# Kernel tuning notes

Measured on AMD Instinct MI355X. Metric: run time of the kernel, lower is better.

## Reference

```python
import jax, jax.numpy as jnp
import numpy as np

EMBED_DIM = 1024
NUM_HEADS = 16
HEAD_DIM = EMBED_DIM // NUM_HEADS
BSZ = 4
SEQ = 1500


def setup_inputs() -> dict:
    key = jax.random.key(0)
    ks = jax.random.split(key, 8)
    s = 0.02
    return {
        "hidden_states": jax.random.normal(ks[0], (BSZ, SEQ, EMBED_DIM), jnp.float32),
        "Wq": jax.random.normal(ks[1], (EMBED_DIM, EMBED_DIM), jnp.float32) * s,
        "bq": jax.random.normal(ks[2], (EMBED_DIM,), jnp.float32) * s,
        "Wk": jax.random.normal(ks[3], (EMBED_DIM, EMBED_DIM), jnp.float32) * s,
        "Wv": jax.random.normal(ks[4], (EMBED_DIM, EMBED_DIM), jnp.float32) * s,
        "bv": jax.random.normal(ks[5], (EMBED_DIM,), jnp.float32) * s,
        "Wo": jax.random.normal(ks[6], (EMBED_DIM, EMBED_DIM), jnp.float32) * s,
        "bo": jax.random.normal(ks[7], (EMBED_DIM,), jnp.float32) * s,
    }


def reference(hidden_states, Wq, bq, Wk, Wv, bv, Wo, bo):
    b, t, e = hidden_states.shape
    h, d = NUM_HEADS, HEAD_DIM
    scaling = d ** -0.5

    def shape(x):  # [b, t, e] -> [b, h, t, d]
        return x.reshape(b, t, h, d).transpose(0, 2, 1, 3)

    # q_proj (with bias) then scale applied to the full projected output,
    # matching the original (scale multiplies q_proj output incl. bias).
    q = shape((hidden_states @ Wq.T + bq) * scaling)
    k = shape(hidden_states @ Wk.T)            # k_proj has no bias in Whisper
    v = shape(hidden_states @ Wv.T + bv)

    # naive materialized attention scores: [b, h, t, t]
    attn_weights = jnp.einsum("bhqd,bhkd->bhqk", q, k)
    attn_probs = jax.nn.softmax(attn_weights, axis=-1)
    attn_output = jnp.einsum("bhqk,bhkd->bhqd", attn_probs, v)

    # [b, h, t, d] -> [b, t, e]
    attn_output = attn_output.transpose(0, 2, 1, 3).reshape(b, t, e)
    return attn_output @ Wo.T + bo
```

## Files before the change

kernel.cpp:

```cpp
#include <hip/hip_runtime.h>
#include <math.h>

#define E 1024
#define NH 16
#define HD 64
#define BSZ_ 4
#define SEQ_ 1500
#define VSTR 1504
#define M_ (BSZ_ * SEQ_)
#define SZE ((size_t)M_ * (size_t)E)
#define QSC (0.125f * 1.44269504f)

#define QA_OFF  0u
#define XB_OFF  6144000u
#define WB_OFF  12288000u
#define WOB_OFF 15433728u
#define VT_OFF  16482304u
#define CVT_TOTAL 10338304u
#define PAD_ELEMS 18432u
#define WS_FAST_BYTES 45289472ull

typedef __attribute__((ext_vector_type(8))) short short8v;
typedef __attribute__((ext_vector_type(4))) float f32x4;
typedef __attribute__((ext_vector_type(16))) float f32x16;
typedef __attribute__((ext_vector_type(4))) unsigned short ushort4v;

__device__ __forceinline__ unsigned short f2bf(float f) {
    union { float f; unsigned int i; } c; c.f = f;
    return (unsigned short)((c.i + 0x7FFFu + ((c.i >> 16) & 1u)) >> 16);
}
__device__ __forceinline__ unsigned int cvt_pk_bf16(float a, float b) {
    unsigned int r;
    asm("v_cvt_pk_bf16_f32 %0, %1, %2" : "=v"(r) : "v"(a), "v"(b));
    return r;
}
__device__ __forceinline__ void perml32(unsigned int &a, unsigned int &b) {
    asm("v_permlane32_swap_b32 %0, %1" : "+v"(a), "+v"(b));
}

__device__ __forceinline__ int swz(int row, int col) {
    return (row << 6) + ((((col >> 3) ^ row) & 7) << 3) + (col & 7);
}
__device__ __forceinline__ int swzf(int r, int d) {
    int row = r >> 1;
    int cs = ((r & 1) << 3) | (d >> 3);
    return row * 128 + ((cs ^ (row & 15)) << 3) + (d & 7);
}

__device__ __forceinline__ short8v pack8(const float* x) {
    union { unsigned int u[4]; short8v v; } r;
    r.u[0] = cvt_pk_bf16(x[0], x[1]);
    r.u[1] = cvt_pk_bf16(x[2], x[3]);
    r.u[2] = cvt_pk_bf16(x[4], x[5]);
    r.u[3] = cvt_pk_bf16(x[6], x[7]);
    return r.v;
}

__device__ __forceinline__ void gload16(const unsigned short* g,
                                        unsigned short* l) {
    __builtin_amdgcn_global_load_lds(
        (const __attribute__((address_space(1))) unsigned int*)(g),
        (__attribute__((address_space(3))) unsigned int*)(l), 16, 0, 0);
}

__global__ __launch_bounds__(256) void cvt_kernel(
    const float* __restrict__ X,  const float* __restrict__ Wk,
    const float* __restrict__ Wv, const float* __restrict__ Wq,
    const float* __restrict__ Wo, unsigned short* __restrict__ ws)
{
    size_t w = ((size_t)blockIdx.x * 256 + threadIdx.x) * 8;
    if (w >= CVT_TOTAL) {
        size_t p0 = w - CVT_TOTAL;
        unsigned short* Vt = ws + VT_OFF;
#pragma unroll
        for (int i = 0; i < 8; ++i) {
            size_t e = p0 + i;
            if (e < 16384u) {
                size_t row = e >> 2;
                Vt[row * VSTR + 1500 + (e & 3)] = 0;
            } else if (e < PAD_ELEMS) {
                Vt[(size_t)4096 * VSTR + (e - 16384u)] = 0;
            }
        }
        return;
    }
    const float* s; unsigned short* d; float sc = 1.0f;
    if (w < 6144000u)      { s = X  + w;             d = ws + XB_OFF + w; }
    else if (w < 7192576u) { s = Wk + (w - 6144000u); d = ws + WB_OFF + (w - 6144000u); }
    else if (w < 8241152u) { s = Wv + (w - 7192576u); d = ws + WB_OFF + 1048576u + (w - 7192576u); }
    else if (w < 9289728u) { s = Wq + (w - 8241152u); d = ws + WB_OFF + 2097152u + (w - 8241152u); sc = QSC; }
    else                   { s = Wo + (w - 9289728u); d = ws + WOB_OFF + (w - 9289728u); }
    float t[8];
    *(float4*)t = *(const float4*)s;
    *(float4*)(t + 4) = *(const float4*)(s + 4);
#pragma unroll
    for (int i = 0; i < 8; ++i) t[i] *= sc;
    *(short8v*)d = pack8(t);
}

__device__ __forceinline__ void gemm128b(
    const unsigned short* __restrict__ Arow,
    const unsigned short* __restrict__ Brow,
    unsigned short* As, unsigned short* Bs, int tid, f32x4 acc[4][4])
{
    const int lane = tid & 63, wid = tid >> 6;
    const int wm = tid >> 7, wn = (tid >> 6) & 1;
    for (int k0 = 0; k0 < E; k0 += 64) {
#pragma unroll
        for (int i = 0; i < 4; ++i) {
            int row = wid * 32 + i * 8 + (lane >> 3);
            int sl = (lane & 7) ^ (row & 7);
            unsigned short* lbase = As + (wid * 32 + i * 8) * 64;
            gload16(Arow + (size_t)row * E + k0 + sl * 8, lbase);
            unsigned short* lbase2 = Bs + (wid * 32 + i * 8) * 64;
            gload16(Brow + (size_t)row * E + k0 + sl * 8, lbase2);
        }
        __syncthreads();
#pragma unroll
        for (int kk = 0; kk < 64; kk += 32) {
            short8v afr[4], bfr[4];
#pragma unroll
            for (int m = 0; m < 4; ++m)
                afr[m] = *(const short8v*)(As + swz(wm * 64 + m * 16 + (lane & 15),
                                                    kk + (lane >> 4) * 8));
#pragma unroll
            for (int n = 0; n < 4; ++n)
                bfr[n] = *(const short8v*)(Bs + swz(wn * 64 + n * 16 + (lane & 15),
                                                    kk + (lane >> 4) * 8));
            __builtin_amdgcn_s_setprio(1);
#pragma unroll
            for (int m = 0; m < 4; ++m)
#pragma unroll
                for (int n = 0; n < 4; ++n)
                    acc[m][n] = __builtin_amdgcn_mfma_f32_16x16x32_bf16(
                        afr[m], bfr[n], acc[m][n], 0, 0, 0);
            __builtin_amdgcn_s_setprio(0);
        }
        __syncthreads();
    }
}

__global__ __launch_bounds__(256) void proj_fast(
    const unsigned short* __restrict__ Xb, const unsigned short* __restrict__ Wb,
    const float* __restrict__ bv, const float* __restrict__ bq,
    unsigned short* __restrict__ Kb, unsigned short* __restrict__ Vt,
    unsigned short* __restrict__ Qa)
{
    __shared__ unsigned short As[128 * 64], Bs[128 * 64];
    const int sid = blockIdx.x;
    const int nid = (sid & 7) * 141 + (sid >> 3);
    const int mb = nid / 24, nb = nid % 24;
    const int z = nb >> 3;
    const size_t m0 = (size_t)mb * 128;
    const int tid = threadIdx.x, lane = tid & 63;
    const int wm = tid >> 7, wn = (tid >> 6) & 1;

    f32x4 acc[4][4];
#pragma unroll
    for (int m = 0; m < 4; ++m)
#pragma unroll
        for (int n = 0; n < 4; ++n)
#pragma unroll
            for (int i = 0; i < 4; ++i) acc[m][n][i] = 0.f;

    gemm128b(Xb + m0 * E, Wb + (size_t)nb * 128 * E, As, Bs, tid, acc);

#pragma unroll
    for (int m = 0; m < 4; ++m) {
        long gi0 = (long)m0 + wm * 64 + m * 16 + (lane >> 4) * 4;
#pragma unroll
        for (int n = 0; n < 4; ++n) {
            int col = (nb & 7) * 128 + wn * 64 + n * 16 + (lane & 15);
            if (z == 0) {
#pragma unroll
                for (int rg = 0; rg < 4; ++rg) {
                    long gi = gi0 + rg;
                    if (gi < M_) Kb[(size_t)gi * E + col] = f2bf(acc[m][n][rg]);
                }
            } else if (z == 2) {
                float bias = bq[col] * QSC;
#pragma unroll
                for (int rg = 0; rg < 4; ++rg) {
                    long gi = gi0 + rg;
                    if (gi < M_)
                        Qa[(size_t)gi * E + col] = f2bf(acc[m][n][rg] + bias);
                }
            } else {
                float bias = bv[col];
                if (gi0 + 3 < M_) {
                    long bb = gi0 / SEQ_, t0 = gi0 % SEQ_;
                    union { unsigned int u[2]; ushort4v v; } pk;
                    pk.u[0] = cvt_pk_bf16(acc[m][n][0] + bias, acc[m][n][1] + bias);
                    pk.u[1] = cvt_pk_bf16(acc[m][n][2] + bias, acc[m][n][3] + bias);
                    *(ushort4v*)(Vt + ((size_t)bb * E + col) * VSTR + t0) = pk.v;
                } else {
#pragma unroll
                    for (int rg = 0; rg < 4; ++rg) {
                        long gi = gi0 + rg;
                        if (gi < M_) {
                            long bb = gi / SEQ_, t = gi % SEQ_;
                            Vt[((size_t)bb * E + col) * VSTR + t] =
                                f2bf(acc[m][n][rg] + bias);
                        }
                    }
                }
            }
        }
    }
}

__global__ __launch_bounds__(256) void oproj_fast(
    const unsigned short* __restrict__ Ab, const unsigned short* __restrict__ Wob,
    const float* __restrict__ bo, float* __restrict__ out)
{
    __shared__ unsigned short As[128 * 64], Bs[128 * 64];
    const int sid = blockIdx.x;
    const int nid = (sid & 7) * 47 + (sid >> 3);
    const int mb = nid >> 3, nb = nid & 7;
    const size_t m0 = (size_t)mb * 128;
    const int tid = threadIdx.x, lane = tid & 63;
    const int wm = tid >> 7, wn = (tid >> 6) & 1;

    f32x4 acc[4][4];
#pragma unroll
    for (int m = 0; m < 4; ++m)
#pragma unroll
        for (int n = 0; n < 4; ++n)
#pragma unroll
            for (int i = 0; i < 4; ++i) acc[m][n][i] = 0.f;

    gemm128b(Ab + m0 * E, Wob + (size_t)nb * 128 * E, As, Bs, tid, acc);

#pragma unroll
    for (int m = 0; m < 4; ++m) {
        long gi0 = (long)m0 + wm * 64 + m * 16 + (lane >> 4) * 4;
#pragma unroll
        for (int n = 0; n < 4; ++n) {
            int col = nb * 128 + wn * 64 + n * 16 + (lane & 15);
            float bias = bo[col];
#pragma unroll
            for (int rg = 0; rg < 4; ++rg) {
                long gi = gi0 + rg;
                if (gi < M_) out[(size_t)gi * E + col] = acc[m][n][rg] + bias;
            }
        }
    }
}

__global__ __launch_bounds__(256, 4) void attn_gl(
    const unsigned short* __restrict__ Kb,
    const unsigned short* __restrict__ Vt,
    unsigned short* __restrict__ Qa)
{
    __shared__ unsigned short ks[4096], vs[4096];
    const int sid = blockIdx.x;
    const int nid = (sid & 7) * 96 + (sid >> 3);
    const int bh = nid / 12, qb = nid % 12;
    const int b = bh >> 4, hh = bh & 15;
    const int tid = threadIdx.x, lane = tid & 63, wz = tid >> 6;
    const int c = lane & 31, g2 = lane >> 5;
    const int q0 = qb * 128 + wz * 32;

    const unsigned short* kbase = Kb + (size_t)b * SEQ_ * E + hh * 64;
    const unsigned short* vbase = Vt + ((size_t)b * E + hh * 64) * VSTR;

    auto stageKV = [&](int kt0) {
#pragma unroll
        for (int i = 0; i < 2; ++i) {
            int j = (i * 4 + wz) * 64 + lane;
            int rp = j >> 4;
            int u = (j & 15) ^ (rp & 15);
            int r = rp * 2 + (u >> 3);
            int s = u & 7;
            gload16(kbase + (size_t)(kt0 + r) * E + s * 8,
                    ks + (i * 4 + wz) * 512);
            gload16(vbase + (size_t)r * VSTR + kt0 + s * 8,
                    vs + (i * 4 + wz) * 512);
        }
    };

    short8v qf[4];
    {
        int qr = q0 + c;
        bool ok = qr < SEQ_;
        const unsigned short* qp = Qa + ((size_t)b * SEQ_ + qr) * E + hh * 64 + 8 * g2;
#pragma unroll
        for (int t = 0; t < 4; ++t) {
            short8v zv;
#pragma unroll
            for (int i = 0; i < 8; ++i) zv[i] = 0;
            if (ok) zv = *(const short8v*)(qp + t * 16);
            qf[t] = zv;
        }
    }

    f32x16 o0, o1;
#pragma unroll
    for (int i = 0; i < 16; ++i) { o0[i] = 0.f; o1[i] = 0.f; }
    float lsum = 0.f;

    const int NT = (SEQ_ + 63) / 64;
    for (int it = 0; it < NT; ++it) {
        const int kt0 = it * 64;
        __syncthreads();
        stageKV(kt0);
        __syncthreads();
        const bool tail = (kt0 + 64 > SEQ_);

#pragma unroll
        for (int nt = 0; nt < 2; ++nt) {
            f32x16 s;
#pragma unroll
            for (int i = 0; i < 16; ++i) s[i] = 0.f;
            __builtin_amdgcn_s_setprio(1);
#pragma unroll
            for (int t = 0; t < 4; ++t) {
                short8v af = *(const short8v*)(ks + swzf(nt * 32 + c, t * 16 + 8 * g2));
                s = __builtin_amdgcn_mfma_f32_32x32x16_bf16(af, qf[t], s, 0, 0, 0);
            }
            __builtin_amdgcn_s_setprio(0);
            if (tail) {
#pragma unroll
                for (int r = 0; r < 16; ++r) {
                    int key = kt0 + nt * 32 + (r & 3) + 8 * (r >> 2) + 4 * g2;
                    if (key >= SEQ_) s[r] = -1e30f;
                }
            }
            unsigned int pk[8];
            float ls0 = 0.f, ls1 = 0.f;
#pragma unroll
            for (int h = 0; h < 8; ++h) {
                float p0 = __builtin_amdgcn_exp2f(s[2 * h]);
                float p1 = __builtin_amdgcn_exp2f(s[2 * h + 1]);
                if (h & 1) ls1 += p0 + p1; else ls0 += p0 + p1;
                pk[h] = cvt_pk_bf16(p0, p1);
            }
            lsum += ls0 + ls1;
            perml32(pk[0], pk[2]); perml32(pk[1], pk[3]);
            perml32(pk[4], pk[6]); perml32(pk[5], pk[7]);
            __builtin_amdgcn_s_setprio(1);
#pragma unroll
            for (int tau = 0; tau < 2; ++tau) {
                union { unsigned int ww[4]; short8v v; } pa;
                pa.ww[0] = pk[4 * tau + 0];
                pa.ww[1] = pk[4 * tau + 1];
                pa.ww[2] = pk[4 * tau + 2];
                pa.ww[3] = pk[4 * tau + 3];
                int t = nt * 2 + tau;
                short8v vb0 = *(const short8v*)(vs + swzf(0 + c, t * 16 + 8 * g2));
                short8v vb1 = *(const short8v*)(vs + swzf(32 + c, t * 16 + 8 * g2));
                o0 = __builtin_amdgcn_mfma_f32_32x32x16_bf16(pa.v, vb0, o0, 0, 0, 0);
                o1 = __builtin_amdgcn_mfma_f32_32x32x16_bf16(pa.v, vb1, o1, 0, 0, 0);
            }
            __builtin_amdgcn_s_setprio(0);
        }
    }

    lsum += __shfl_xor(lsum, 32, 64);
    __syncthreads();
    float* lf = (float*)ks + wz * 32;
    if (lane < 32) lf[c] = 1.0f / lsum;
#pragma unroll
    for (int r = 0; r < 16; ++r) {
        int ql = (r & 3) + 8 * (r >> 2) + 4 * g2;
        int tq = q0 + ql;
        if (tq < SEQ_) {
            float inv = lf[ql];
            unsigned short* op = Qa + ((size_t)b * SEQ_ + tq) * E + hh * 64;
            op[c] = f2bf(o0[r] * inv);
            op[32 + c] = f2bf(o1[r] * inv);
        }
    }
}

template <bool ABF>
__device__ __forceinline__ void gemm128(
    const float* __restrict__ Af, const unsigned short* __restrict__ Ab,
    size_t arow0, int avalid,
    const float* __restrict__ W, int wrow0,
    unsigned short* As, unsigned short* Bs,
    int tid, f32x4 acc[4][4])
{
    const int lane = tid & 63;
    const int wm = (tid >> 7), wn = (tid >> 6) & 1;
    float4 pA[8]; short8v pAb[4]; float4 pB[8];

    auto loadT = [&](int k0) {
#pragma unroll
        for (int uu = 0; uu < 4; ++uu) {
            int u = tid + uu * 256, row = u >> 3, sl = (u & 7) * 8;
            if constexpr (ABF) {
                short8v t;
#pragma unroll
                for (int i = 0; i < 8; ++i) t[i] = 0;
                if (row < avalid)
                    t = *(const short8v*)(Ab + (arow0 + row) * E + k0 + sl);
                pAb[uu] = t;
            } else {
                float4 x0 = make_float4(0.f, 0.f, 0.f, 0.f), x1 = x0;
                if (row < avalid) {
                    const float* p = Af + (arow0 + row) * (size_t)E + k0 + sl;
                    x0 = *(const float4*)p; x1 = *(const float4*)(p + 4);
                }
                pA[2 * uu] = x0; pA[2 * uu + 1] = x1;
            }
            const float* q = W + (size_t)(wrow0 + row) * E + k0 + sl;
            pB[2 * uu] = *(const float4*)q;
            pB[2 * uu + 1] = *(const float4*)(q + 4);
        }
    };
    auto commitT = [&]() {
#pragma unroll
        for (int uu = 0; uu < 4; ++uu) {
            int u = tid + uu * 256, row = u >> 3, sl = (u & 7) * 8;
            if constexpr (ABF) {
                *(short8v*)(As + swz(row, sl)) = pAb[uu];
            } else {
                float t[8];
                *(float4*)t = pA[2 * uu]; *(float4*)(t + 4) = pA[2 * uu + 1];
                *(short8v*)(As + swz(row, sl)) = pack8(t);
            }
            float t2[8];
            *(float4*)t2 = pB[2 * uu]; *(float4*)(t2 + 4) = pB[2 * uu + 1];
            *(short8v*)(Bs + swz(row, sl)) = pack8(t2);
        }
    };

    loadT(0);
    for (int k0 = 0; k0 < E; k0 += 64) {
        __syncthreads();
        commitT();
        __syncthreads();
        if (k0 + 64 < E) loadT(k0 + 64);
#pragma unroll
        for (int kk = 0; kk < 64; kk += 32) {
            short8v afr[4], bfr[4];
#pragma unroll
            for (int m = 0; m < 4; ++m)
                afr[m] = *(const short8v*)(As + swz(wm * 64 + m * 16 + (lane & 15),
                                                    kk + (lane >> 4) * 8));
#pragma unroll
            for (int n = 0; n < 4; ++n)
                bfr[n] = *(const short8v*)(Bs + swz(wn * 64 + n * 16 + (lane & 15),
                                                    kk + (lane >> 4) * 8));
            __builtin_amdgcn_s_setprio(1);
#pragma unroll
            for (int m = 0; m < 4; ++m)
#pragma unroll
                for (int n = 0; n < 4; ++n)
                    acc[m][n] = __builtin_amdgcn_mfma_f32_16x16x32_bf16(
                        afr[m], bfr[n], acc[m][n], 0, 0, 0);
            __builtin_amdgcn_s_setprio(0);
        }
    }
}

__global__ __launch_bounds__(256, 2) void proj_kernel(
    const float* __restrict__ X, const float* __restrict__ Wk,
    const float* __restrict__ Wv, const float* __restrict__ bv,
    const float* __restrict__ Wq, const float* __restrict__ bq,
    unsigned short* __restrict__ Kb, unsigned short* __restrict__ Vt,
    unsigned short* __restrict__ Qo)
{
    __shared__ unsigned short As[128 * 64], Bs[128 * 64];
    const int sid = blockIdx.x, cpx = gridDim.x >> 3;
    const int nid = (sid & 7) * cpx + (sid >> 3);
    const int mb = nid / 24, nb = nid % 24;
    const int z = nb >> 3, nbz = nb & 7;
    const size_t m0 = (size_t)mb * 128;
    const int avalid = (M_ - (int)m0) < 128 ? (M_ - (int)m0) : 128;
    const float* W = (z == 0) ? Wk : (z == 1) ? Wv : Wq;

    f32x4 acc[4][4];
#pragma unroll
    for (int m = 0; m < 4; ++m)
#pragma unroll
        for (int n = 0; n < 4; ++n)
#pragma unroll
            for (int i = 0; i < 4; ++i) acc[m][n][i] = 0.f;

    gemm128<false>(X, nullptr, m0, avalid, W, nbz * 128, As, Bs, threadIdx.x, acc);

    const int tid = threadIdx.x, lane = tid & 63;
    const int wm = (tid >> 7), wn = (tid >> 6) & 1;
#pragma unroll
    for (int m = 0; m < 4; ++m) {
        long gi0 = (long)m0 + wm * 64 + m * 16 + (lane >> 4) * 4;
#pragma unroll
        for (int n = 0; n < 4; ++n) {
            int col = nbz * 128 + wn * 64 + n * 16 + (lane & 15);
            if (z == 0) {
#pragma unroll
                for (int rg = 0; rg < 4; ++rg) {
                    long gi = gi0 + rg;
                    if (gi < M_) Kb[(size_t)gi * E + col] = f2bf(acc[m][n][rg]);
                }
            } else if (z == 2) {
                float bias = bq[col];
#pragma unroll
                for (int rg = 0; rg < 4; ++rg) {
                    long gi = gi0 + rg;
                    if (gi < M_)
                        Qo[(size_t)gi * E + col] = f2bf((acc[m][n][rg] + bias) * QSC);
                }
            } else {
                float bias = bv[col];
                if (gi0 + 3 < M_) {
                    long bb = gi0 / SEQ_, t0 = gi0 % SEQ_;
                    union { unsigned int u[2]; ushort4v v; } pk;
                    pk.u[0] = cvt_pk_bf16(acc[m][n][0] + bias, acc[m][n][1] + bias);
                    pk.u[1] = cvt_pk_bf16(acc[m][n][2] + bias, acc[m][n][3] + bias);
                    *(ushort4v*)(Vt + ((size_t)bb * E + col) * SEQ_ + t0) = pk.v;
                } else {
#pragma unroll
                    for (int rg = 0; rg < 4; ++rg) {
                        long gi = gi0 + rg;
                        if (gi < M_) {
                            long bb = gi / SEQ_, t = gi % SEQ_;
                            Vt[((size_t)bb * E + col) * SEQ_ + t] =
                                f2bf(acc[m][n][rg] + bias);
                        }
                    }
                }
            }
        }
    }
}

__global__ __launch_bounds__(256, 2) void oproj_kernel(
    const unsigned short* __restrict__ Ab, const float* __restrict__ Wo,
    const float* __restrict__ bo, float* __restrict__ out)
{
    __shared__ unsigned short As[128 * 64], Bs[128 * 64];
    const int sid = blockIdx.x, cpx = gridDim.x >> 3;
    const int nid = (sid & 7) * cpx + (sid >> 3);
    const int mb = nid >> 3, nb = nid & 7;
    const size_t m0 = (size_t)mb * 128;
    const int avalid = (M_ - (int)m0) < 128 ? (M_ - (int)m0) : 128;

    f32x4 acc[4][4];
#pragma unroll
    for (int m = 0; m < 4; ++m)
#pragma unroll
        for (int n = 0; n < 4; ++n)
#pragma unroll
            for (int i = 0; i < 4; ++i) acc[m][n][i] = 0.f;

    gemm128<true>(nullptr, Ab, m0, avalid, Wo, nb * 128, As, Bs, threadIdx.x, acc);

    const int tid = threadIdx.x, lane = tid & 63;
    const int wm = (tid >> 7), wn = (tid >> 6) & 1;
#pragma unroll
    for (int m = 0; m < 4; ++m) {
        long gi0 = (long)m0 + wm * 64 + m * 16 + (lane >> 4) * 4;
#pragma unroll
        for (int n = 0; n < 4; ++n) {
            int col = nb * 128 + wn * 64 + n * 16 + (lane & 15);
            float bias = bo[col];
#pragma unroll
            for (int rg = 0; rg < 4; ++rg) {
                long gi = gi0 + rg;
                if (gi < M_) out[(size_t)gi * E + col] = acc[m][n][rg] + bias;
            }
        }
    }
}

__global__ __launch_bounds__(256, 4) void attn_fallback(
    const unsigned short* __restrict__ Kb,
    const unsigned short* __restrict__ Vt,
    unsigned short* __restrict__ Qa)
{
    __shared__ unsigned short ks[2][32 * 128], vs[2][32 * 128];
    const int sid = blockIdx.x;
    const int nid = (sid & 7) * 96 + (sid >> 3);
    const int bh = nid / 12, qb = nid % 12;
    const int b = bh >> 4, hh = bh & 15;
    const int tid = threadIdx.x, lane = tid & 63, wz = tid >> 6;
    const int c = lane & 31, g2 = lane >> 5;
    const int q0 = qb * 128 + wz * 32;

    const unsigned short* kbase = Kb + (size_t)b * SEQ_ * E + hh * 64;
    const unsigned short* vbase = Vt + ((size_t)b * E + hh * 64) * SEQ_;

    short8v kreg[2];
    ushort4v vreg[4];
    auto loadK = [&](int kt0) {
#pragma unroll
        for (int uu = 0; uu < 2; ++uu) {
            int u = tid + uu * 256, key = u >> 3, slot = (u & 7) * 8;
            short8v t;
#pragma unroll
            for (int i = 0; i < 8; ++i) t[i] = 0;
            int gk = kt0 + key;
            if (gk < SEQ_) t = *(const short8v*)(kbase + (size_t)gk * E + slot);
            kreg[uu] = t;
        }
    };
    auto loadV = [&](int kt0) {
#pragma unroll
        for (int uu = 0; uu < 4; ++uu) {
            int u = tid + uu * 256, d = u >> 4, q4 = (u & 15) * 4;
            ushort4v t; t[0] = t[1] = t[2] = t[3] = 0;
            int col = kt0 + q4, rem = SEQ_ - col;
            const unsigned short* src = vbase + (size_t)d * SEQ_ + col;
            if (rem >= 4) t = *(const ushort4v*)src;
            else if (rem > 0) { for (int e2 = 0; e2 < 4; ++e2) if (e2 < rem) t[e2] = src[e2]; }
            vreg[uu] = t;
        }
    };
    auto commitKV = [&](unsigned short* kd, unsigned short* vd) {
#pragma unroll
        for (int uu = 0; uu < 2; ++uu) {
            int u = tid + uu * 256;
            *(short8v*)(kd + swzf(u >> 3, (u & 7) * 8)) = kreg[uu];
        }
#pragma unroll
        for (int uu = 0; uu < 4; ++uu) {
            int u = tid + uu * 256;
            *(ushort4v*)(vd + swzf(u >> 4, (u & 15) * 4)) = vreg[uu];
        }
    };

    loadK(0); loadV(0);

    short8v qf[4];
    {
        int qr = q0 + c;
        bool ok = qr < SEQ_;
        const unsigned short* qp = Qa + ((size_t)b * SEQ_ + qr) * E + hh * 64 + 8 * g2;
#pragma unroll
        for (int t = 0; t < 4; ++t) {
            short8v zv;
#pragma unroll
            for (int i = 0; i < 8; ++i) zv[i] = 0;
            if (ok) zv = *(const short8v*)(qp + t * 16);
            qf[t] = zv;
        }
    }

    f32x16 o0, o1;
#pragma unroll
    for (int i = 0; i < 16; ++i) { o0[i] = 0.f; o1[i] = 0.f; }
    float lsum = 0.f;

    commitKV(ks[0], vs[0]);
    __syncthreads();
    loadK(64); loadV(64);

    const int NT = (SEQ_ + 63) / 64;
    for (int it = 0; it < NT; ++it) {
        const int kt0 = it * 64;
        const unsigned short* kcur = ks[it & 1];
        const unsigned short* vcur = vs[it & 1];
        const bool tail = (kt0 + 64 > SEQ_);

#pragma unroll
        for (int nt = 0; nt < 2; ++nt) {
            f32x16 s;
#pragma unroll
            for (int i = 0; i < 16; ++i) s[i] = 0.f;
#pragma unroll
            for (int t = 0; t < 4; ++t) {
                short8v af = *(const short8v*)(kcur + swzf(nt * 32 + c, t * 16 + 8 * g2));
                s = __builtin_amdgcn_mfma_f32_32x32x16_bf16(af, qf[t], s, 0, 0, 0);
            }
            if (tail) {
#pragma unroll
                for (int r = 0; r < 16; ++r) {
                    int key = kt0 + nt * 32 + (r & 3) + 8 * (r >> 2) + 4 * g2;
                    if (key >= SEQ_) s[r] = -1e30f;
                }
            }
            unsigned int pk[8];
            float ls0 = 0.f, ls1 = 0.f;
#pragma unroll
            for (int h = 0; h < 8; ++h) {
                float p0 = __builtin_amdgcn_exp2f(s[2 * h]);
                float p1 = __builtin_amdgcn_exp2f(s[2 * h + 1]);
                if (h & 1) ls1 += p0 + p1; else ls0 += p0 + p1;
                pk[h] = cvt_pk_bf16(p0, p1);
            }
            lsum += ls0 + ls1;
            perml32(pk[0], pk[2]); perml32(pk[1], pk[3]);
            perml32(pk[4], pk[6]); perml32(pk[5], pk[7]);
#pragma unroll
            for (int tau = 0; tau < 2; ++tau) {
                union { unsigned int ww[4]; short8v v; } pa;
                pa.ww[0] = pk[4 * tau + 0];
                pa.ww[1] = pk[4 * tau + 1];
                pa.ww[2] = pk[4 * tau + 2];
                pa.ww[3] = pk[4 * tau + 3];
                int t = nt * 2 + tau;
                short8v vb0 = *(const short8v*)(vcur + swzf(0 + c, t * 16 + 8 * g2));
                short8v vb1 = *(const short8v*)(vcur + swzf(32 + c, t * 16 + 8 * g2));
                o0 = __builtin_amdgcn_mfma_f32_32x32x16_bf16(pa.v, vb0, o0, 0, 0, 0);
                o1 = __builtin_amdgcn_mfma_f32_32x32x16_bf16(pa.v, vb1, o1, 0, 0, 0);
            }
        }

        if (it + 1 < NT) {
            commitKV(ks[(it + 1) & 1], vs[(it + 1) & 1]);
            __syncthreads();
            if (it + 2 < NT) { loadK(kt0 + 128); loadV(kt0 + 128); }
        }
    }

    lsum += __shfl_xor(lsum, 32, 64);
    __syncthreads();
    float* lf = (float*)ks[0] + wz * 32;
    if (lane < 32) lf[c] = 1.0f / lsum;
#pragma unroll
    for (int r = 0; r < 16; ++r) {
        int ql = (r & 3) + 8 * (r >> 2) + 4 * g2;
        int tq = q0 + ql;
        if (tq < SEQ_) {
            float inv = lf[ql];
            unsigned short* op = Qa + ((size_t)b * SEQ_ + tq) * E + hh * 64;
            op[c] = f2bf(o0[r] * inv);
            op[32 + c] = f2bf(o1[r] * inv);
        }
    }
}

extern "C" void kernel_launch(void* const* d_in, const int* in_sizes, int n_in,
                              void* d_out, int out_size, void* d_ws, size_t ws_size,
                              hipStream_t stream) {
    const float* hs = (const float*)d_in[0];
    const float* Wq = (const float*)d_in[1];
    const float* bq = (const float*)d_in[2];
    const float* Wk = (const float*)d_in[3];
    const float* Wv = (const float*)d_in[4];
    const float* bv = (const float*)d_in[5];
    const float* Wo = (const float*)d_in[6];
    const float* bo = (const float*)d_in[7];

    unsigned short* Kb = (unsigned short*)d_out;
    unsigned short* ws = (unsigned short*)d_ws;
    unsigned short* Qa = ws + QA_OFF;
    float* out = (float*)d_out;

    if (ws_size >= WS_FAST_BYTES) {
        unsigned short* Vt = ws + VT_OFF;
        cvt_kernel<<<dim3(5057), 256, 0, stream>>>(hs, Wk, Wv, Wq, Wo, ws);
        proj_fast<<<dim3(1128), 256, 0, stream>>>(ws + XB_OFF, ws + WB_OFF,
                                                  bv, bq, Kb, Vt, Qa);
        attn_gl<<<dim3(768), 256, 0, stream>>>(Kb, Vt, Qa);
        oproj_fast<<<dim3(376), 256, 0, stream>>>(Qa, ws + WOB_OFF, bo, out);
    } else {
        unsigned short* Vt = (unsigned short*)d_out + SZE;
        proj_kernel<<<dim3(47 * 24), 256, 0, stream>>>(hs, Wk, Wv, bv, Wq, bq,
                                                       Kb, Vt, Qa);
        attn_fallback<<<dim3(768), 256, 0, stream>>>(Kb, Vt, Qa);
        oproj_kernel<<<dim3(47 * 8), 256, 0, stream>>>(Qa, Wo, bo, out);
    }
}
```

Baseline: 160.4 us.

## Double-buffer LDS staging in projection GEMMs and attention K/V loop

The shared projection GEMM is rewritten to use two LDS buffers with a 32-wide K step. The next tile is prefetched with global_load_lds while MFMAs run on the current tile, and a new swizzle matches the 32-column layout. The attention kernel likewise ping-pongs K/V tiles, prefetching the next 64-key block before computing on the current one and dropping one barrier per iteration. This aims to hide global-memory latency behind MFMA work. The cost is doubled LDS use in attention, and in the GEMMs twice as many loop iterations and barriers.

Result: faster. 146.2 us, median of 3 (-8.8%).

```diff
diff --git a/kernel.cpp b/kernel.cpp
--- a/kernel.cpp
+++ b/kernel.cpp
@@ -41,6 +41,9 @@
 __device__ __forceinline__ int swz(int row, int col) {
     return (row << 6) + ((((col >> 3) ^ row) & 7) << 3) + (col & 7);
 }
+__device__ __forceinline__ int swz32(int r, int c) {
+    return r * 32 + ((((c >> 3) ^ (r >> 1)) & 3) << 3) + (c & 7);
+}
 __device__ __forceinline__ int swzf(int r, int d) {
     int row = r >> 1;
     int cs = ((r & 1) << 3) | (d >> 3);
@@ -98,45 +101,57 @@
     *(short8v*)d = pack8(t);
 }
 
-__device__ __forceinline__ void gemm128b(
+__device__ __forceinline__ void stage32(const unsigned short* __restrict__ Row,
+                                        unsigned short* lbuf, int k0,
+                                        int wv, int lane) {
+#pragma unroll
+    for (int g = 0; g < 2; ++g) {
+        int j = g * 256 + wv * 64 + lane;
+        int r = j >> 2;
+        int s = (j & 3) ^ ((r >> 1) & 3);
+        gload16(Row + (size_t)r * E + k0 + s * 8,
+                lbuf + (size_t)(g * 256 + wv * 64) * 8);
+    }
+}
+
+__device__ __forceinline__ void gemm128db(
     const unsigned short* __restrict__ Arow,
     const unsigned short* __restrict__ Brow,
-    unsigned short* As, unsigned short* Bs, int tid, f32x4 acc[4][4])
-{
-    const int lane = tid & 63, wid = tid >> 6;
+    unsigned short* As, unsigned short* Bs,
+    int tid, f32x4 acc[4][4])
+{
+    const int lane = tid & 63, wv = tid >> 6;
     const int wm = tid >> 7, wn = (tid >> 6) & 1;
-    for (int k0 = 0; k0 < E; k0 += 64) {
-#pragma unroll
-        for (int i = 0; i < 4; ++i) {
-            int row = wid * 32 + i * 8 + (lane >> 3);
-            int sl = (lane & 7) ^ (row & 7);
-            unsigned short* lbase = As + (wid * 32 + i * 8) * 64;
-            gload16(Arow + (size_t)row * E + k0 + sl * 8, lbase);
-            unsigned short* lbase2 = Bs + (wid * 32 + i * 8) * 64;
-            gload16(Brow + (size_t)row * E + k0 + sl * 8, lbase2);
-        }
+    stage32(Arow, As, 0, wv, lane);
+    stage32(Brow, Bs, 0, wv, lane);
+    __syncthreads();
+    int buf = 0;
+    for (int k0 = 0; k0 < E; k0 += 32) {
+        if (k0 + 32 < E) {
+            stage32(Arow, As + (buf ^ 1) * 4096, k0 + 32, wv, lane);
+            stage32(Brow, Bs + (buf ^ 1) * 4096, k0 + 32, wv, lane);
+        }
+        const unsigned short* Ab = As + buf * 4096;
+        const unsigned short* Bb = Bs + buf * 4096;
+        short8v afr[4], bfr[4];
+#pragma unroll
+        for (int m = 0; m < 4; ++m)
+            afr[m] = *(const short8v*)(Ab + swz32(wm * 64 + m * 16 + (lane & 15),
+                                                  (lane >> 4) * 8));
+#pragma unroll
+        for (int n = 0; n < 4; ++n)
+            bfr[n] = *(const short8v*)(Bb + swz32(wn * 64 + n * 16 + (lane & 15),
+                                                  (lane >> 4) * 8));
+        __builtin_amdgcn_s_setprio(1);
+#pragma unroll
+        for (int m = 0; m < 4; ++m)
+#pragma unroll
+            for (int n = 0; n < 4; ++n)
+                acc[m][n] = __builtin_amdgcn_mfma_f32_16x16x32_bf16(
+                    afr[m], bfr[n], acc[m][n], 0, 0, 0);
+        __builtin_amdgcn_s_setprio(0);
         __syncthreads();
-#pragma unroll
-        for (int kk = 0; kk < 64; kk += 32) {
-            short8v afr[4], bfr[4];
-#pragma unroll
-            for (int m = 0; m < 4; ++m)
-                afr[m] = *(const short8v*)(As + swz(wm * 64 + m * 16 + (lane & 15),
-                                                    kk + (lane >> 4) * 8));
-#pragma unroll
-            for (int n = 0; n < 4; ++n)
-                bfr[n] = *(const short8v*)(Bs + swz(wn * 64 + n * 16 + (lane & 15),
-                                                    kk + (lane >> 4) * 8));
-            __builtin_amdgcn_s_setprio(1);
-#pragma unroll
-            for (int m = 0; m < 4; ++m)
-#pragma unroll
-                for (int n = 0; n < 4; ++n)
-                    acc[m][n] = __builtin_amdgcn_mfma_f32_16x16x32_bf16(
-                        afr[m], bfr[n], acc[m][n], 0, 0, 0);
-            __builtin_amdgcn_s_setprio(0);
-        }
-        __syncthreads();
+        buf ^= 1;
     }
 }
 
@@ -146,7 +161,7 @@
     unsigned short* __restrict__ Kb, unsigned short* __restrict__ Vt,
     unsigned short* __restrict__ Qa)
 {
-    __shared__ unsigned short As[128 * 64], Bs[128 * 64];
+    __shared__ unsigned short As[2 * 128 * 32], Bs[2 * 128 * 32];
     const int sid = blockIdx.x;
     const int nid = (sid & 7) * 141 + (sid >> 3);
     const int mb = nid / 24, nb = nid % 24;
@@ -163,7 +178,7 @@
 #pragma unroll
             for (int i = 0; i < 4; ++i) acc[m][n][i] = 0.f;
 
-    gemm128b(Xb + m0 * E, Wb + (size_t)nb * 128 * E, As, Bs, tid, acc);
+    gemm128db(Xb + m0 * E, Wb + (size_t)nb * 128 * E, As, Bs, tid, acc);
 
 #pragma unroll
     for (int m = 0; m < 4; ++m) {
@@ -213,7 +228,7 @@
     const unsigned short* __restrict__ Ab, const unsigned short* __restrict__ Wob,
     const float* __restrict__ bo, float* __restrict__ out)
 {
-    __shared__ unsigned short As[128 * 64], Bs[128 * 64];
+    __shared__ unsigned short As[2 * 128 * 32], Bs[2 * 128 * 32];
     const int sid = blockIdx.x;
     const int nid = (sid & 7) * 47 + (sid >> 3);
     const int mb = nid >> 3, nb = nid & 7;
@@ -229,7 +244,7 @@
 #pragma unroll
             for (int i = 0; i < 4; ++i) acc[m][n][i] = 0.f;
 
-    gemm128b(Ab + m0 * E, Wob + (size_t)nb * 128 * E, As, Bs, tid, acc);
+    gemm128db(Ab + m0 * E, Wob + (size_t)nb * 128 * E, As, Bs, tid, acc);
 
 #pragma unroll
     for (int m = 0; m < 4; ++m) {
@@ -252,7 +267,7 @@
     const unsigned short* __restrict__ Vt,
     unsigned short* __restrict__ Qa)
 {
-    __shared__ unsigned short ks[4096], vs[4096];
+    __shared__ unsigned short ks[2][4096], vs[2][4096];
     const int sid = blockIdx.x;
     const int nid = (sid & 7) * 96 + (sid >> 3);
     const int bh = nid / 12, qb = nid % 12;
@@ -264,7 +279,7 @@
     const unsigned short* kbase = Kb + (size_t)b * SEQ_ * E + hh * 64;
     const unsigned short* vbase = Vt + ((size_t)b * E + hh * 64) * VSTR;
 
-    auto stageKV = [&](int kt0) {
+    auto stageKV = [&](int bf, int kt0) {
 #pragma unroll
         for (int i = 0; i < 2; ++i) {
             int j = (i * 4 + wz) * 64 + lane;
@@ -273,9 +288,9 @@
             int r = rp * 2 + (u >> 3);
             int s = u & 7;
             gload16(kbase + (size_t)(kt0 + r) * E + s * 8,
-                    ks + (i * 4 + wz) * 512);
+                    ks[bf] + (i * 4 + wz) * 512);
             gload16(vbase + (size_t)r * VSTR + kt0 + s * 8,
-                    vs + (i * 4 + wz) * 512);
+                    vs[bf] + (i * 4 + wz) * 512);
         }
     };
 
@@ -299,13 +314,17 @@
     for (int i = 0; i < 16; ++i) { o0[i] = 0.f; o1[i] = 0.f; }
     float lsum = 0.f;
 
+    stageKV(0, 0);
+    __syncthreads();
+    int buf = 0;
+
     const int NT = (SEQ_ + 63) / 64;
     for (int it = 0; it < NT; ++it) {
         const int kt0 = it * 64;
-        __syncthreads();
-        stageKV(kt0);
-        __syncthreads();
+        if (it + 1 < NT) stageKV(buf ^ 1, kt0 + 64);
         const bool tail = (kt0 + 64 > SEQ_);
+        const unsigned short* kcur = ks[buf];
+        const unsigned short* vcur = vs[buf];
 
 #pragma unroll
         for (int nt = 0; nt < 2; ++nt) {
@@ -315,7 +334,7 @@
             __builtin_amdgcn_s_setprio(1);
 #pragma unroll
             for (int t = 0; t < 4; ++t) {
-                short8v af = *(const short8v*)(ks + swzf(nt * 32 + c, t * 16 + 8 * g2));
+                short8v af = *(const short8v*)(kcur + swzf(nt * 32 + c, t * 16 + 8 * g2));
                 s = __builtin_amdgcn_mfma_f32_32x32x16_bf16(af, qf[t], s, 0, 0, 0);
             }
             __builtin_amdgcn_s_setprio(0);
@@ -347,18 +366,21 @@
                 pa.ww[2] = pk[4 * tau + 2];
                 pa.ww[3] = pk[4 * tau + 3];
                 int t = nt * 2 + tau;
-                short8v vb0 = *(const short8v*)(vs + swzf(0 + c, t * 16 + 8 * g2));
-                short8v vb1 = *(const short8v*)(vs + swzf(32 + c, t * 16 + 8 * g2));
+                short8v vb0 = *(const short8v*)(vcur + swzf(0 + c, t * 16 + 8 * g2));
+                short8v vb1 = *(const short8v*)(vcur + swzf(32 + c, t * 16 + 8 * g2));
                 o0 = __builtin_amdgcn_mfma_f32_32x32x16_bf16(pa.v, vb0, o0, 0, 0, 0);
                 o1 = __builtin_amdgcn_mfma_f32_32x32x16_bf16(pa.v, vb1, o1, 0, 0, 0);
             }
             __builtin_amdgcn_s_setprio(0);
         }
+
+        __syncthreads();
+        buf ^= 1;
     }
 
     lsum += __shfl_xor(lsum, 32, 64);
     __syncthreads();
-    float* lf = (float*)ks + wz * 32;
+    float* lf = (float*)ks[0] + wz * 32;
     if (lane < 32) lf[c] = 1.0f / lsum;
 #pragma unroll
     for (int r = 0; r < 16; ++r) {
```
